# Performance work log

Hardware: AMD Instinct MI355X
Metric: run time of the kernel (lower is better)

## Reference

```python
import jax, jax.numpy as jnp
import numpy as np

D_MODEL = 1024
N_HEADS = 16
D_K = D_MODEL // N_HEADS
SCALE = 1.0 / np.sqrt(D_K)


def _bayes_linear(x, w_mu, w_rho, b_mu, b_rho):
    """Closed-form mean/variance of a variational linear layer."""
    w_sig = jax.nn.softplus(w_rho)
    b_sig = jax.nn.softplus(b_rho)
    mean = x @ w_mu.T + b_mu
    var = (x * x) @ (w_sig * w_sig).T + b_sig * b_sig
    return mean, var


def setup_inputs() -> dict:
    key = jax.random.key(0)
    ks = jax.random.split(key, 12)
    B, N, d_raw = 8, 1024, 16
    inp = {
        "H": jax.random.normal(ks[0], (B, N, D_MODEL), dtype=jnp.float32),
        "x_raw": jax.random.normal(ks[1], (B, N, d_raw), dtype=jnp.float32),
    }
    # kaiming_normal fan_in linear -> std = 1/sqrt(fan_in)
    std = 1.0 / np.sqrt(D_MODEL)
    for i, name in enumerate(["q", "k", "v", "o"]):
        inp[f"W{name}_mu"] = jax.random.normal(ks[2 + i], (D_MODEL, D_MODEL), dtype=jnp.float32) * std
        inp[f"W{name}_rho"] = jnp.full((D_MODEL, D_MODEL), -3.0, dtype=jnp.float32)
        inp[f"b{name}_mu"] = jnp.zeros((D_MODEL,), dtype=jnp.float32)
        inp[f"b{name}_rho"] = jnp.full((D_MODEL,), -3.0, dtype=jnp.float32)
    inp["log_sigma_f"] = jnp.zeros((N_HEADS,), dtype=jnp.float32)
    inp["log_length"] = jnp.zeros((N_HEADS,), dtype=jnp.float32)
    return inp


def reference(H, x_raw,
              Wq_mu, Wq_rho, bq_mu, bq_rho,
              Wk_mu, Wk_rho, bk_mu, bk_rho,
              Wv_mu, Wv_rho, bv_mu, bv_rho,
              Wo_mu, Wo_rho, bo_mu, bo_rho,
              log_sigma_f, log_length):
    B, N, _ = H.shape

    # Q/K variances are computed but discarded in the original forward; skip them.
    Q = H @ Wq_mu.T + bq_mu
    K = H @ Wk_mu.T + bk_mu
    V, V_v = _bayes_linear(H, Wv_mu, Wv_rho, bv_mu, bv_rho)

    def split_heads(t):  # [B,N,D] -> [B,H,N,dk]
        return t.reshape(B, N, N_HEADS, D_K).transpose(0, 2, 1, 3)

    Q, K, V, V_v = split_heads(Q), split_heads(K), split_heads(V), split_heads(V_v)

    scores = jnp.einsum("bhnd,bhmd->bhnm", Q, K) * SCALE

    # RBF kernel on raw inputs, added per head
    sigma_f2 = jnp.exp(2.0 * log_sigma_f)            # [H]
    length2 = jnp.exp(2.0 * log_length)              # [H]
    x2 = jnp.sum(x_raw * x_raw, axis=-1)             # [B,N]
    dist2 = jnp.maximum(
        x2[:, :, None] + x2[:, None, :] - 2.0 * jnp.einsum("bnd,bmd->bnm", x_raw, x_raw),
        0.0,
    )                                                # [B,N,N]
    rbf = sigma_f2[None, :, None, None] * jnp.exp(
        -dist2[:, None, :, :] / (2.0 * length2[None, :, None, None])
    )                                                # [B,H,N,N]
    scores = scores + rbf

    attn = jax.nn.softmax(scores, axis=-1)           # dropout is identity in eval

    context = jnp.einsum("bhnm,bhmd->bhnd", attn, V)
    context = context.transpose(0, 2, 1, 3).reshape(B, N, D_MODEL)
    var_attn = jnp.einsum("bhnm,bhmd->bhnd", attn * attn, V_v)
    var_attn = var_attn.transpose(0, 2, 1, 3).reshape(B, N, D_MODEL)

    out_mean, out_var_proj = _bayes_linear(context, Wo_mu, Wo_rho, bo_mu, bo_rho)
    out_var = out_var_proj + var_attn
    return out_mean, out_var
```

## Files before the change

### kernel.cpp

```cpp
#include <hip/hip_runtime.h>
#include <hip/hip_bf16.h>
#include <stdint.h>


#define D_MODEL 1024
#define NSEQ    1024
#define BATCH   8
#define NHEADS  16
#define DK      64
#define TOK     8192

typedef _Float16  h8  __attribute__((ext_vector_type(8)));
typedef _Float16  h4  __attribute__((ext_vector_type(4)));
typedef _Float16  h2v __attribute__((ext_vector_type(2)));
typedef __fp16    g2  __attribute__((ext_vector_type(2)));
typedef float     f4  __attribute__((ext_vector_type(4)));

__device__ __forceinline__ f4 mfma_h(h8 a, h8 b, f4 c){
  return __builtin_amdgcn_mfma_f32_16x16x32_f16(a, b, c, 0, 0, 0);
}

__device__ __forceinline__ h2v pk_f16(float a, float b){
  g2 t = __builtin_amdgcn_cvt_pkrtz(a, b);
  return __builtin_bit_cast(h2v, t);
}

__device__ __forceinline__ void async_copy16(void* lds, const void* g){
  __builtin_amdgcn_global_load_lds(
      (const __attribute__((address_space(1))) unsigned int*)(uintptr_t)g,
      (__attribute__((address_space(3))) unsigned int*)(unsigned int)(uintptr_t)lds,
      16, 0, 0);
}

__device__ __forceinline__ float softplusf(float x){
  return (x > 20.f) ? x : log1pf(__expf(x));
}

__global__ __launch_bounds__(256) void prep_all(
    const float* __restrict__ Wq, const float* __restrict__ Wk,
    const float* __restrict__ Wv, const float* __restrict__ Wvr,
    const float* __restrict__ Wo, const float* __restrict__ Wor,
    const float* __restrict__ H, const float* __restrict__ x,
    _Float16* __restrict__ Wcat, _Float16* __restrict__ Wocat,
    _Float16* __restrict__ Hh, _Float16* __restrict__ H2h,
    _Float16* __restrict__ xk, _Float16* __restrict__ xq)
{
  const int bid = blockIdx.x;
  if (bid < 6144){
    const int seg = bid >> 10;
    const int i   = ((bid & 1023)*256 + threadIdx.x)*4;
    const float* src = seg==0 ? Wq : seg==1 ? Wk : seg==2 ? Wv : seg==3 ? Wvr : seg==4 ? Wo : Wor;
    _Float16* dst = (seg < 4) ? (Wcat + (size_t)seg*1048576)
                              : (Wocat + (size_t)(seg-4)*1048576);
    const bool sp2 = (seg==3) || (seg==5);
    float4 v = *(const float4*)(src + i);
    float vv[4] = {v.x, v.y, v.z, v.w};
    #pragma unroll
    for (int j=0;j<4;j++){
      float f = vv[j];
      if (sp2){ float s = softplusf(f); f = s*s; }
      dst[i+j] = (_Float16)f;
    }
  } else if (bid < 14336){
    int i = ((bid - 6144)*256 + threadIdx.x)*4;
    float4 v = *(const float4*)(H + i);
    float vv[4] = {v.x, v.y, v.z, v.w};
    #pragma unroll
    for (int j=0;j<4;j++){
      Hh[i+j]  = (_Float16)vv[j];
      H2h[i+j] = (_Float16)(vv[j]*vv[j]);
    }
  } else {
    int t = (bid - 14336)*256 + threadIdx.x;
    const float* p = x + (size_t)t*16;
    _Float16 a[32], bb[32];
    float s = 0.f;
    #pragma unroll
    for (int j=0;j<16;j++){
      float f = p[j];
      a[j]  = (_Float16)f;
      bb[j] = (_Float16)(2.f*f);
      s += f*f;
    }
    _Float16 shi = (_Float16)s;
    _Float16 slo = (_Float16)(s - (float)shi);
    a[16]=shi; a[17]=slo; a[18]=(_Float16)1.f; a[19]=(_Float16)1.f;
    bb[16]=(_Float16)-1.f; bb[17]=(_Float16)-1.f; bb[18]=-shi; bb[19]=-slo;
    #pragma unroll
    for (int j=20;j<32;j++){ a[j]=(_Float16)0.f; bb[j]=(_Float16)0.f; }
    #pragma unroll
    for (int j=0;j<4;j++){
      *(h8*)(xk + (size_t)t*32 + j*8) = *(const h8*)&a[j*8];
      *(h8*)(xq + (size_t)t*32 + j*8) = *(const h8*)&bb[j*8];
    }
  }
}

template<int MODE>
__global__ __launch_bounds__(256) void gemm_fused(
    const _Float16* __restrict__ A0, const _Float16* __restrict__ A1,
    const _Float16* __restrict__ Wcat,
    const float* __restrict__ bias0, const float* __restrict__ bias1,
    const float* __restrict__ bias2, const float* __restrict__ bias3,
    _Float16* __restrict__ Qo, _Float16* __restrict__ Ko,
    _Float16* __restrict__ Vto, _Float16* __restrict__ Vvto,
    float* __restrict__ meanO, float* __restrict__ varO)
{
  constexpr int NBN = (MODE==0) ? 32 : 16;
  __shared__ _Float16 smem[32768];
  _Float16* sA = smem;
  _Float16* sB = smem + 16384;
  const int tid = threadIdx.x;
  const int lane = tid & 63;
  const int wid  = tid >> 6;
  const int wm = wid >> 1, wn = wid & 1;
  const int l15 = lane & 15, l4 = lane >> 4;
  const int bid = blockIdx.x;
  const int x   = bid & 7;
  const int idx = bid >> 3;
  const int grp = idx >> 6;
  const int inr = idx & 63;
  const int bm  = (x << 3) + (inr & 7);
  const int bn  = (grp << 3) + (inr >> 3);
  const int row0 = bm << 7, col0 = bn << 7;
  const int seg = col0 >> 10;

  const _Float16* A = (MODE==0) ? (seg < 3 ? A0 : A1) : A0;
  const bool sqA = (MODE==1) && (seg==1);
  const _Float16* B = Wcat + (size_t)col0 * 1024;

  f4 acc[4][4];
  #pragma unroll
  for (int i=0;i<4;i++)
    #pragma unroll
    for (int j=0;j<4;j++)
      #pragma unroll
      for (int r=0;r<4;r++) acc[i][j][r] = 0.f;

  for (int kt = 0; kt < 1024; kt += 128){
    __syncthreads();
    #pragma unroll
    for (int k=0;k<8;k++){
      int c  = tid + k*256;
      int rg = c >> 4, ch = c & 15;
      int sw = ((ch ^ (rg & 15)) << 3);
      async_copy16(&sA[c*8], A + (size_t)(row0+rg)*1024 + kt + sw);
      async_copy16(&sB[c*8], B + (size_t)rg*1024 + kt + sw);
    }
    __syncthreads();

    #pragma unroll
    for (int ks=0; ks<4; ks++){
      h8 a[4], b[4];
      #pragma unroll
      for (int mf=0; mf<4; mf++){
        int r  = (wm<<6) + (mf<<4) + l15;
        int ck = (ks*4 + l4) ^ (r & 15);
        a[mf] = *(const h8*)&sA[r*128 + ck*8];
        if (sqA) a[mf] = a[mf]*a[mf];
      }
      #pragma unroll
      for (int nf=0; nf<4; nf++){
        int r  = (wn<<6) + (nf<<4) + l15;
        int ck = (ks*4 + l4) ^ (r & 15);
        b[nf] = *(const h8*)&sB[r*128 + ck*8];
      }
      #pragma unroll
      for (int mf=0; mf<4; mf++)
        #pragma unroll
        for (int nf=0; nf<4; nf++)
          acc[mf][nf] = mfma_h(a[mf], b[nf], acc[mf][nf]);
    }
  }

  if (MODE==0 && seg >= 2){
    _Float16* T = (seg==2) ? Vto : Vvto;
    const size_t tbase = ((size_t)(row0>>10)<<20)
                       + (size_t)(col0 & 1023)*1024 + (row0 & 1023);
    const int o  = tid >> 1;
    const int hf = tid & 1;
    #pragma unroll
    for (int rh=0; rh<2; rh++){
      __syncthreads();
      if (wm == rh){
        #pragma unroll
        for (int nf=0; nf<4; nf++){
          int col = (wn<<6) + (nf<<4) + l15;
          float bb2 = (seg==2) ? bias2[(col0 + col) & 1023]
                               : bias3[(col0 + col) & 1023];
          float bv;
          if (seg==3){ float s = softplusf(bb2); bv = s*s; } else bv = bb2;
          #pragma unroll
          for (int mf=0; mf<4; mf++){
            int n   = (mf<<4) + (l4<<2);
            int nsw = n ^ ((col & 7) << 3);
            h4 hv;
            #pragma unroll
            for (int r=0;r<4;r++) hv[r] = (_Float16)(acc[mf][nf][r] + bv);
            *(h4*)&smem[col*64 + nsw] = hv;
          }
        }
      }
      __syncthreads();
      #pragma unroll
      for (int j=0; j<4; j++){
        int n   = hf*8 + j*16;
        int nsw = n ^ ((o & 7) << 3);
        h8 v = *(const h8*)&smem[o*64 + nsw];
        *(h8*)(T + tbase + (size_t)o*1024 + rh*64 + n) = v;
      }
    }
    return;
  }

  const float* bias = (seg==0) ? bias0 : bias1;
  const bool sp2 = (MODE==1) && (seg==1);
  const float CQK = 0.18033688f;

  #pragma unroll
  for (int nf=0; nf<4; nf++){
    int colg = col0 + (wn<<6) + (nf<<4) + l15;
    int colm = colg & 1023;
    float bb = bias[colm];
    float bv = sp2 ? ({ float s = softplusf(bb); s*s; }) : bb;
    #pragma unroll
    for (int mf=0; mf<4; mf++){
      int rbase = row0 + (wm<<6) + (mf<<4) + (l4<<2);
      #pragma unroll
      for (int r=0;r<4;r++){
        int row = rbase + r;
        float v = acc[mf][nf][r] + bv;
        if (MODE==0){
          if (seg==0) Qo[(size_t)row*1024 + colm] = (_Float16)(v * CQK);
          else        Ko[(size_t)row*1024 + colm] = (_Float16)v;
        } else {
          size_t idxo = (size_t)row*1024 + colm;
          if (seg==0) meanO[idxo] = v;
          else        varO[idxo] = v + varO[idxo];
        }
      }
    }
  }
}

__global__ __launch_bounds__(256, 2) void attn_kernel(
    const _Float16* __restrict__ Qh, const _Float16* __restrict__ Kh,
    const _Float16* __restrict__ Vt, const _Float16* __restrict__ Vvt,
    const _Float16* __restrict__ xk, const _Float16* __restrict__ xq,
    const float* __restrict__ log_sigma_f, const float* __restrict__ log_length,
    _Float16* __restrict__ ctx_out, float* __restrict__ var_out)
{
  const int bid = blockIdx.x;
  const int swz = (bid & 7) * 128 + (bid >> 3);
  const int qt = swz & 7;
  const int bh = swz >> 3;
  const int b  = bh >> 4, h = bh & 15;
  const int tid = threadIdx.x;
  const int lane = tid & 63, wid = tid >> 6;
  const int l15 = lane & 15, l4 = lane >> 4;
  const float L2E   = 1.44269504f;
  const float sig2l = __expf(2.f*log_sigma_f[h]) * L2E;
  const float e2c   = 0.5f*__expf(-2.f*log_length[h]) * L2E;

  __shared__ _Float16 sK[2][4096];
  __shared__ _Float16 sV[2][4096];
  __shared__ _Float16 sVv[2][4096];

  const int t0 = b*NSEQ + qt*128;
  const int wq = wid*32;

  int krow_[4];
  #pragma unroll
  for (int fm=0; fm<4; fm++)
    krow_[fm] = ((fm&1)<<2) + (l15&3) + ((l15>>2)<<3) + ((fm>>1)<<5);

  h8 qf[2][2];
  #pragma unroll
  for (int fq=0; fq<2; fq++)
    #pragma unroll
    for (int ks=0; ks<2; ks++){
      size_t off = (size_t)(t0 + wq + fq*16 + l15)*D_MODEL + h*DK + ks*32 + l4*8;
      qf[fq][ks] = *(const h8*)(Qh + off);
    }
  const _Float16 e2ch = (_Float16)e2c;
  h8 xqf[2];
  #pragma unroll
  for (int fq=0; fq<2; fq++){
    xqf[fq] = *(const h8*)(xq + (size_t)(t0 + wq + fq*16 + l15)*32 + l4*8);
    xqf[fq] = xqf[fq] * e2ch;
  }

  h8 ones;
  #pragma unroll
  for (int j=0;j<8;j++) ones[j] = (_Float16)1.f;

  float mrun[2] = {-1e30f, -1e30f};
  f4 lacc[2], ctx[2][4], var[2][4];
  #pragma unroll
  for (int fq=0; fq<2; fq++){
    #pragma unroll
    for (int r=0;r<4;r++) lacc[fq][r] = 0.f;
    #pragma unroll
    for (int fd=0; fd<4; fd++)
      #pragma unroll
      for (int r=0;r<4;r++){ ctx[fq][fd][r] = 0.f; var[fq][fd][r] = 0.f; }
  }

  auto stage = [&](int bi, int mt){
    #pragma unroll
    for (int k=0;k<6;k++){
      int c = tid + k*256;
      if (k < 2){
        int rg = c >> 3, ch = c & 7;
        int g  = (rg & 3) | (((rg >> 3) & 1) << 2);
        int sw = ((ch ^ g) << 3);
        async_copy16(&sK[bi][c*8], Kh + (size_t)(b*NSEQ + mt + rg)*D_MODEL + h*DK + sw);
      } else if (k < 4){
        int cc = c - 512; int rg = cc >> 3, sw = (((cc & 7) ^ (rg & 7)) << 3);
        async_copy16(&sV[bi][cc*8], Vt + ((size_t)b << 20) + (size_t)(h*DK + rg)*NSEQ + mt + sw);
      } else {
        int cc = c - 1024; int rg = cc >> 3, sw = (((cc & 7) ^ (rg & 7)) << 3);
        async_copy16(&sVv[bi][cc*8], Vvt + ((size_t)b << 20) + (size_t)(h*DK + rg)*NSEQ + mt + sw);
      }
    }
  };

  h8 xkf[4], xknxt[4];
  #pragma unroll
  for (int fm=0; fm<4; fm++)
    xkf[fm] = *(const h8*)(xk + (size_t)(b*NSEQ + krow_[fm])*32 + l4*8);

  stage(0, 0);
  __syncthreads();

  for (int it = 0; it < NSEQ/64; it++){
    const int bi = it & 1;
    const int mt = it*64;
    if (it + 1 < NSEQ/64){
      stage(bi^1, mt + 64);
      #pragma unroll
      for (int fm=0; fm<4; fm++)
        xknxt[fm] = *(const h8*)(xk + (size_t)(b*NSEQ + mt + 64 + krow_[fm])*32 + l4*8);
    }

    f4 S[2][4];
    #pragma unroll
    for (int fm=0; fm<4; fm++){
      const int krow = krow_[fm];
      const int g    = (krow & 3) | (((krow >> 3) & 1) << 2);
      h8 kb0 = *(const h8*)&sK[bi][krow*64 + ((l4      ^ g))*8];
      h8 kb1 = *(const h8*)&sK[bi][krow*64 + (((4+l4) ^ g))*8];
      #pragma unroll
      for (int fq=0; fq<2; fq++){
        f4 s, xd;
        #pragma unroll
        for (int r=0;r<4;r++){ s[r]=0.f; xd[r]=0.f; }
        s  = mfma_h(kb0, qf[fq][0], s);
        s  = mfma_h(kb1, qf[fq][1], s);
        xd = mfma_h(xkf[fm], xqf[fq], xd);
        #pragma unroll
        for (int r=0;r<4;r++)
          S[fq][fm][r] = s[r] + sig2l*__builtin_amdgcn_exp2f(xd[r]);
      }
    }

    h8 pa[2][2];
    #pragma unroll
    for (int fq=0; fq<2; fq++){
      float tm = S[fq][0][0];
      #pragma unroll
      for (int fm=0; fm<4; fm++)
        #pragma unroll
        for (int r=0;r<4;r++) tm = fmaxf(tm, S[fq][fm][r]);
      tm = fmaxf(tm, __shfl_xor(tm, 16));
      tm = fmaxf(tm, __shfl_xor(tm, 32));
      int nd = tm > mrun[fq] + 5.7708f;
      if (__any(nd)){
        float mn = fmaxf(mrun[fq], tm);
        float sc = __builtin_amdgcn_exp2f(mrun[fq] - mn);
        mrun[fq] = mn;
        float scr[4];
        #pragma unroll
        for (int r=0;r<4;r++) scr[r] = __shfl(sc, (l4<<2) + r);
        #pragma unroll
        for (int r=0;r<4;r++) lacc[fq][r] *= scr[r];
        #pragma unroll
        for (int fd=0; fd<4; fd++)
          #pragma unroll
          for (int r=0;r<4;r++){
            ctx[fq][fd][r] *= scr[r];
            var[fq][fd][r] *= scr[r]*scr[r];
          }
      }
      #pragma unroll
      for (int ks=0; ks<2; ks++){
        h2v q0 = pk_f16(__builtin_amdgcn_exp2f(S[fq][2*ks][0] - mrun[fq]),
                        __builtin_amdgcn_exp2f(S[fq][2*ks][1] - mrun[fq]));
        h2v q1 = pk_f16(__builtin_amdgcn_exp2f(S[fq][2*ks][2] - mrun[fq]),
                        __builtin_amdgcn_exp2f(S[fq][2*ks][3] - mrun[fq]));
        h2v q2 = pk_f16(__builtin_amdgcn_exp2f(S[fq][2*ks+1][0] - mrun[fq]),
                        __builtin_amdgcn_exp2f(S[fq][2*ks+1][1] - mrun[fq]));
        h2v q3 = pk_f16(__builtin_amdgcn_exp2f(S[fq][2*ks+1][2] - mrun[fq]),
                        __builtin_amdgcn_exp2f(S[fq][2*ks+1][3] - mrun[fq]));
        pa[fq][ks] = (h8){q0[0],q0[1],q1[0],q1[1],q2[0],q2[1],q3[0],q3[1]};
      }
    }

    #pragma unroll
    for (int ks=0; ks<2; ks++){
      h8 pa2[2];
      #pragma unroll
      for (int fq=0; fq<2; fq++){
        pa2[fq] = pa[fq][ks]*pa[fq][ks];
        lacc[fq] = mfma_h(pa[fq][ks], ones, lacc[fq]);
      }
      #pragma unroll
      for (int fd=0; fd<4; fd++){
        int drow = fd*16 + l15;
        int ck = (ks*4 + l4) ^ (drow & 7);
        h8 vb  = *(const h8*)&sV[bi][drow*64 + ck*8];
        h8 vvb = *(const h8*)&sVv[bi][drow*64 + ck*8];
        #pragma unroll
        for (int fq=0; fq<2; fq++){
          ctx[fq][fd] = mfma_h(pa[fq][ks], vb,  ctx[fq][fd]);
          var[fq][fd] = mfma_h(pa2[fq],    vvb, var[fq][fd]);
        }
      }
    }
    __syncthreads();
    #pragma unroll
    for (int fm=0; fm<4; fm++) xkf[fm] = xknxt[fm];
  }

  #pragma unroll
  for (int fq=0; fq<2; fq++)
    #pragma unroll
    for (int r=0;r<4;r++){
      int t = t0 + wq + fq*16 + l4*4 + r;
      float linv = 1.f / lacc[fq][r];
      size_t base = (size_t)t*D_MODEL + h*DK + l15;
      float c[4];
      #pragma unroll
      for (int fd=0; fd<4; fd++) c[fd] = ctx[fq][fd][r] * linv;
      #pragma unroll
      for (int fd=0; fd<4; fd++) ctx_out[base + fd*16] = (_Float16)c[fd];
      #pragma unroll
      for (int fd=0; fd<4; fd++) var_out[base + fd*16] = var[fq][fd][r] * linv * linv;
    }
}


extern "C" void kernel_launch(void* const* d_in, const int* in_sizes, int n_in,
                              void* d_out, int out_size, void* d_ws, size_t ws_size,
                              hipStream_t stream){
  (void)in_sizes; (void)n_in; (void)out_size; (void)ws_size;
  const float* H      = (const float*)d_in[0];
  const float* x_raw  = (const float*)d_in[1];
  const float* Wq_mu  = (const float*)d_in[2];
  const float* bq_mu  = (const float*)d_in[4];
  const float* Wk_mu  = (const float*)d_in[6];
  const float* bk_mu  = (const float*)d_in[8];
  const float* Wv_mu  = (const float*)d_in[10];
  const float* Wv_rho = (const float*)d_in[11];
  const float* bv_mu  = (const float*)d_in[12];
  const float* bv_rho = (const float*)d_in[13];
  const float* Wo_mu  = (const float*)d_in[14];
  const float* Wo_rho = (const float*)d_in[15];
  const float* bo_mu  = (const float*)d_in[16];
  const float* bo_rho = (const float*)d_in[17];
  const float* lsf    = (const float*)d_in[18];
  const float* lln    = (const float*)d_in[19];

  char* ws = (char*)d_ws;
  const size_t MB = 1024*1024;
  _Float16* Hh    = (_Float16*)(ws + 0*MB);
  _Float16* H2h   = (_Float16*)(ws + 16*MB);
  _Float16* Wcat  = (_Float16*)(ws + 32*MB);
  _Float16* Wocat = (_Float16*)(ws + 40*MB);
  _Float16* Qh    = (_Float16*)(ws + 46*MB);
  _Float16* Kh    = (_Float16*)(ws + 62*MB);
  _Float16* Vt    = (_Float16*)(ws + 78*MB);
  _Float16* Vvt   = (_Float16*)(ws + 94*MB);
  _Float16* ctxh  = (_Float16*)(ws + 110*MB);
  _Float16* xk    = (_Float16*)(ws + 142*MB);
  _Float16* xqb   = (_Float16*)(ws + 142*MB + 512*1024);

  float* out_mean = (float*)d_out;
  float* out_var  = out_mean + (size_t)TOK*D_MODEL;

  prep_all<<<14368, 256, 0, stream>>>(Wq_mu, Wk_mu, Wv_mu, Wv_rho, Wo_mu, Wo_rho,
      H, x_raw, Wcat, Wocat, Hh, H2h, xk, xqb);

  gemm_fused<0><<<2048, 256, 0, stream>>>(Hh, H2h, Wcat,
      bq_mu, bk_mu, bv_mu, bv_rho,
      Qh, Kh, Vt, Vvt, nullptr, nullptr);

  attn_kernel<<<1024, 256, 0, stream>>>(Qh, Kh, Vt, Vvt, xk, xqb, lsf, lln,
      ctxh, out_var);

  gemm_fused<1><<<1024, 256, 0, stream>>>(ctxh, nullptr, Wocat,
      bo_mu, bo_rho, nullptr, nullptr,
      nullptr, nullptr, nullptr, nullptr, out_mean, out_var);
}
```

Measured before the change: 247.5 us.

## Use 8 waves per attention block with 16 query rows per wave

The attention kernel moves from 4 waves each handling 32 query rows to 8 waves each handling 16 rows, and launches 512 threads per block. The aim is to cut per-wave register pressure and raise occupancy, with each wave owning fewer accumulators and the K/V tile staging spread across more threads. In exchange, each K/V fragment loaded from LDS now feeds half as many MFMAs, so LDS read traffic per FLOP doubles, and more waves wait at each barrier.

```diff
diff --git a/kernel.cpp b/kernel.cpp
--- a/kernel.cpp
+++ b/kernel.cpp
@@ -243,7 +243,7 @@
   }
 }
 
-__global__ __launch_bounds__(256, 2) void attn_kernel(
+__global__ __launch_bounds__(512, 4) void attn_kernel(
     const _Float16* __restrict__ Qh, const _Float16* __restrict__ Kh,
     const _Float16* __restrict__ Vt, const _Float16* __restrict__ Vvt,
     const _Float16* __restrict__ xk, const _Float16* __restrict__ xq,
@@ -267,55 +267,46 @@
   __shared__ _Float16 sVv[2][4096];
 
   const int t0 = b*NSEQ + qt*128;
-  const int wq = wid*32;
+  const int wq = wid*16;
 
   int krow_[4];
   #pragma unroll
   for (int fm=0; fm<4; fm++)
     krow_[fm] = ((fm&1)<<2) + (l15&3) + ((l15>>2)<<3) + ((fm>>1)<<5);
 
-  h8 qf[2][2];
-  #pragma unroll
-  for (int fq=0; fq<2; fq++)
-    #pragma unroll
-    for (int ks=0; ks<2; ks++){
-      size_t off = (size_t)(t0 + wq + fq*16 + l15)*D_MODEL + h*DK + ks*32 + l4*8;
-      qf[fq][ks] = *(const h8*)(Qh + off);
-    }
+  h8 qf[2];
+  #pragma unroll
+  for (int ks=0; ks<2; ks++){
+    size_t off = (size_t)(t0 + wq + l15)*D_MODEL + h*DK + ks*32 + l4*8;
+    qf[ks] = *(const h8*)(Qh + off);
+  }
   const _Float16 e2ch = (_Float16)e2c;
-  h8 xqf[2];
-  #pragma unroll
-  for (int fq=0; fq<2; fq++){
-    xqf[fq] = *(const h8*)(xq + (size_t)(t0 + wq + fq*16 + l15)*32 + l4*8);
-    xqf[fq] = xqf[fq] * e2ch;
-  }
+  h8 xqf = *(const h8*)(xq + (size_t)(t0 + wq + l15)*32 + l4*8);
+  xqf = xqf * e2ch;
 
   h8 ones;
   #pragma unroll
   for (int j=0;j<8;j++) ones[j] = (_Float16)1.f;
 
-  float mrun[2] = {-1e30f, -1e30f};
-  f4 lacc[2], ctx[2][4], var[2][4];
-  #pragma unroll
-  for (int fq=0; fq<2; fq++){
-    #pragma unroll
-    for (int r=0;r<4;r++) lacc[fq][r] = 0.f;
-    #pragma unroll
-    for (int fd=0; fd<4; fd++)
-      #pragma unroll
-      for (int r=0;r<4;r++){ ctx[fq][fd][r] = 0.f; var[fq][fd][r] = 0.f; }
-  }
+  float mrun = -1e30f;
+  f4 lacc, ctx[4], var[4];
+  #pragma unroll
+  for (int r=0;r<4;r++) lacc[r] = 0.f;
+  #pragma unroll
+  for (int fd=0; fd<4; fd++)
+    #pragma unroll
+    for (int r=0;r<4;r++){ ctx[fd][r] = 0.f; var[fd][r] = 0.f; }
 
   auto stage = [&](int bi, int mt){
     #pragma unroll
-    for (int k=0;k<6;k++){
-      int c = tid + k*256;
-      if (k < 2){
+    for (int k=0;k<3;k++){
+      int c = tid + k*512;
+      if (c < 512){
         int rg = c >> 3, ch = c & 7;
         int g  = (rg & 3) | (((rg >> 3) & 1) << 2);
         int sw = ((ch ^ g) << 3);
         async_copy16(&sK[bi][c*8], Kh + (size_t)(b*NSEQ + mt + rg)*D_MODEL + h*DK + sw);
-      } else if (k < 4){
+      } else if (c < 1024){
         int cc = c - 512; int rg = cc >> 3, sw = (((cc & 7) ^ (rg & 7)) << 3);
         async_copy16(&sV[bi][cc*8], Vt + ((size_t)b << 20) + (size_t)(h*DK + rg)*NSEQ + mt + sw);
       } else {
@@ -343,88 +334,75 @@
         xknxt[fm] = *(const h8*)(xk + (size_t)(b*NSEQ + mt + 64 + krow_[fm])*32 + l4*8);
     }
 
-    f4 S[2][4];
+    f4 S[4];
     #pragma unroll
     for (int fm=0; fm<4; fm++){
       const int krow = krow_[fm];
       const int g    = (krow & 3) | (((krow >> 3) & 1) << 2);
       h8 kb0 = *(const h8*)&sK[bi][krow*64 + ((l4      ^ g))*8];
       h8 kb1 = *(const h8*)&sK[bi][krow*64 + (((4+l4) ^ g))*8];
-      #pragma unroll
-      for (int fq=0; fq<2; fq++){
-        f4 s, xd;
+      f4 s, xd;
+      #pragma unroll
+      for (int r=0;r<4;r++){ s[r]=0.f; xd[r]=0.f; }
+      s  = mfma_h(kb0, qf[0], s);
+      s  = mfma_h(kb1, qf[1], s);
+      xd = mfma_h(xkf[fm], xqf, xd);
+      #pragma unroll
+      for (int r=0;r<4;r++)
+        S[fm][r] = s[r] + sig2l*__builtin_amdgcn_exp2f(xd[r]);
+    }
+
+    float tm = S[0][0];
+    #pragma unroll
+    for (int fm=0; fm<4; fm++)
+      #pragma unroll
+      for (int r=0;r<4;r++) tm = fmaxf(tm, S[fm][r]);
+    tm = fmaxf(tm, __shfl_xor(tm, 16));
+    tm = fmaxf(tm, __shfl_xor(tm, 32));
+    int nd = tm > mrun + 5.7708f;
+    if (__any(nd)){
+      float mn = fmaxf(mrun, tm);
+      float sc = __builtin_amdgcn_exp2f(mrun - mn);
+      mrun = mn;
+      float scr[4];
+      #pragma unroll
+      for (int r=0;r<4;r++) scr[r] = __shfl(sc, (l4<<2) + r);
+      #pragma unroll
+      for (int r=0;r<4;r++) lacc[r] *= scr[r];
+      #pragma unroll
+      for (int fd=0; fd<4; fd++)
         #pragma unroll
-        for (int r=0;r<4;r++){ s[r]=0.f; xd[r]=0.f; }
-        s  = mfma_h(kb0, qf[fq][0], s);
-        s  = mfma_h(kb1, qf[fq][1], s);
-        xd = mfma_h(xkf[fm], xqf[fq], xd);
-        #pragma unroll
-        for (int r=0;r<4;r++)
-          S[fq][fm][r] = s[r] + sig2l*__builtin_amdgcn_exp2f(xd[r]);
-      }
-    }
-
-    h8 pa[2][2];
-    #pragma unroll
-    for (int fq=0; fq<2; fq++){
-      float tm = S[fq][0][0];
-      #pragma unroll
-      for (int fm=0; fm<4; fm++)
-        #pragma unroll
-        for (int r=0;r<4;r++) tm = fmaxf(tm, S[fq][fm][r]);
-      tm = fmaxf(tm, __shfl_xor(tm, 16));
-      tm = fmaxf(tm, __shfl_xor(tm, 32));
-      int nd = tm > mrun[fq] + 5.7708f;
-      if (__any(nd)){
-        float mn = fmaxf(mrun[fq], tm);
-        float sc = __builtin_amdgcn_exp2f(mrun[fq] - mn);
-        mrun[fq] = mn;
-        float scr[4];
-        #pragma unroll
-        for (int r=0;r<4;r++) scr[r] = __shfl(sc, (l4<<2) + r);
-        #pragma unroll
-        for (int r=0;r<4;r++) lacc[fq][r] *= scr[r];
-        #pragma unroll
-        for (int fd=0; fd<4; fd++)
-          #pragma unroll
-          for (int r=0;r<4;r++){
-            ctx[fq][fd][r] *= scr[r];
-            var[fq][fd][r] *= scr[r]*scr[r];
-          }
-      }
-      #pragma unroll
-      for (int ks=0; ks<2; ks++){
-        h2v q0 = pk_f16(__builtin_amdgcn_exp2f(S[fq][2*ks][0] - mrun[fq]),
-                        __builtin_amdgcn_exp2f(S[fq][2*ks][1] - mrun[fq]));
-        h2v q1 = pk_f16(__builtin_amdgcn_exp2f(S[fq][2*ks][2] - mrun[fq]),
-                        __builtin_amdgcn_exp2f(S[fq][2*ks][3] - mrun[fq]));
-        h2v q2 = pk_f16(__builtin_amdgcn_exp2f(S[fq][2*ks+1][0] - mrun[fq]),
-                        __builtin_amdgcn_exp2f(S[fq][2*ks+1][1] - mrun[fq]));
-        h2v q3 = pk_f16(__builtin_amdgcn_exp2f(S[fq][2*ks+1][2] - mrun[fq]),
-                        __builtin_amdgcn_exp2f(S[fq][2*ks+1][3] - mrun[fq]));
-        pa[fq][ks] = (h8){q0[0],q0[1],q1[0],q1[1],q2[0],q2[1],q3[0],q3[1]};
-      }
-    }
-
+        for (int r=0;r<4;r++){
+          ctx[fd][r] *= scr[r];
+          var[fd][r] *= scr[r]*scr[r];
+        }
+    }
+    h8 pa[2];
     #pragma unroll
     for (int ks=0; ks<2; ks++){
-      h8 pa2[2];
-      #pragma unroll
-      for (int fq=0; fq<2; fq++){
-        pa2[fq] = pa[fq][ks]*pa[fq][ks];
-        lacc[fq] = mfma_h(pa[fq][ks], ones, lacc[fq]);
-      }
+      h2v q0 = pk_f16(__builtin_amdgcn_exp2f(S[2*ks][0] - mrun),
+                      __builtin_amdgcn_exp2f(S[2*ks][1] - mrun));
+      h2v q1 = pk_f16(__builtin_amdgcn_exp2f(S[2*ks][2] - mrun),
+                      __builtin_amdgcn_exp2f(S[2*ks][3] - mrun));
+      h2v q2 = pk_f16(__builtin_amdgcn_exp2f(S[2*ks+1][0] - mrun),
+                      __builtin_amdgcn_exp2f(S[2*ks+1][1] - mrun));
+      h2v q3 = pk_f16(__builtin_amdgcn_exp2f(S[2*ks+1][2] - mrun),
+                      __builtin_amdgcn_exp2f(S[2*ks+1][3] - mrun));
+      pa[ks] = (h8){q0[0],q0[1],q1[0],q1[1],q2[0],q2[1],q3[0],q3[1]};
+    }
+
+    #pragma unroll
+    for (int ks=0; ks<2; ks++){
+      h8 pa2 = pa[ks]*pa[ks];
+      lacc = mfma_h(pa[ks], ones, lacc);
       #pragma unroll
       for (int fd=0; fd<4; fd++){
         int drow = fd*16 + l15;
         int ck = (ks*4 + l4) ^ (drow & 7);
         h8 vb  = *(const h8*)&sV[bi][drow*64 + ck*8];
         h8 vvb = *(const h8*)&sVv[bi][drow*64 + ck*8];
-        #pragma unroll
-        for (int fq=0; fq<2; fq++){
-          ctx[fq][fd] = mfma_h(pa[fq][ks], vb,  ctx[fq][fd]);
-          var[fq][fd] = mfma_h(pa2[fq],    vvb, var[fq][fd]);
-        }
+        ctx[fd] = mfma_h(pa[ks], vb,  ctx[fd]);
+        var[fd] = mfma_h(pa2,    vvb, var[fd]);
       }
     }
     __syncthreads();
@@ -433,20 +411,18 @@
   }
 
   #pragma unroll
-  for (int fq=0; fq<2; fq++)
-    #pragma unroll
-    for (int r=0;r<4;r++){
-      int t = t0 + wq + fq*16 + l4*4 + r;
-      float linv = 1.f / lacc[fq][r];
-      size_t base = (size_t)t*D_MODEL + h*DK + l15;
-      float c[4];
-      #pragma unroll
-      for (int fd=0; fd<4; fd++) c[fd] = ctx[fq][fd][r] * linv;
-      #pragma unroll
-      for (int fd=0; fd<4; fd++) ctx_out[base + fd*16] = (_Float16)c[fd];
-      #pragma unroll
-      for (int fd=0; fd<4; fd++) var_out[base + fd*16] = var[fq][fd][r] * linv * linv;
-    }
+  for (int r=0;r<4;r++){
+    int t = t0 + wq + l4*4 + r;
+    float linv = 1.f / lacc[r];
+    size_t base = (size_t)t*D_MODEL + h*DK + l15;
+    float c[4];
+    #pragma unroll
+    for (int fd=0; fd<4; fd++) c[fd] = ctx[fd][r] * linv;
+    #pragma unroll
+    for (int fd=0; fd<4; fd++) ctx_out[base + fd*16] = (_Float16)c[fd];
+    #pragma unroll
+    for (int fd=0; fd<4; fd++) var_out[base + fd*16] = var[fd][r] * linv * linv;
+  }
 }
 
 
@@ -495,7 +471,7 @@
       bq_mu, bk_mu, bv_mu, bv_rho,
       Qh, Kh, Vt, Vvt, nullptr, nullptr);
 
-  attn_kernel<<<1024, 256, 0, stream>>>(Qh, Kh, Vt, Vvt, xk, xqb, lsf, lln,
+  attn_kernel<<<1024, 512, 0, stream>>>(Qh, Kh, Vt, Vvt, xk, xqb, lsf, lln,
       ctxh, out_var);
 
   gemm_fused<1><<<1024, 256, 0, stream>>>(ctxh, nullptr, Wocat,
```

New measurement: 253.9 us. +2.6%, slower.
